# Kernel optimization log

Hardware: AMD Instinct MI355X
Metric: run time of the kernel (lower is better)

The kernel has to match this reference:

```python
import jax, jax.numpy as jnp
import numpy as np

B, N, IN_DIM = 2, 2048, 512
D_MODEL, N_HEADS, N_CLASSES = 1024, 16, 1024


def sin_pos_encoding(n, d):
    # Matches SinPositionalEncoding buffer pe[:n]
    pos = jnp.arange(n, dtype=jnp.float32)[:, None]
    div = jnp.exp(jnp.arange(0, d, 2, dtype=jnp.float32) * (-np.log(10000.0) / d))
    pe = jnp.zeros((n, d), dtype=jnp.float32)
    pe = pe.at[:, 0::2].set(jnp.sin(pos * div))
    pe = pe.at[:, 1::2].set(jnp.cos(pos * div))
    return pe


def setup_inputs() -> dict:
    key = jax.random.key(0)
    ks = jax.random.split(key, 9)
    s_emb = (2.0 / (IN_DIM + D_MODEL)) ** 0.5
    s_qk = (2.0 / (2 * D_MODEL)) ** 0.5
    s_v = (2.0 / (D_MODEL + 1)) ** 0.5
    s_o = (2.0 / (N_HEADS + D_MODEL)) ** 0.5
    s_dec = (2.0 / (D_MODEL + N_CLASSES)) ** 0.5
    return {
        'X': jax.random.normal(ks[0], (B, N, IN_DIM), dtype=jnp.float32),
        'emb_w': jax.random.normal(ks[1], (IN_DIM, D_MODEL), dtype=jnp.float32) * s_emb,
        'emb_b': jax.random.normal(ks[2], (D_MODEL,), dtype=jnp.float32) * 0.01,
        'Wq': jax.random.normal(ks[3], (N_HEADS, D_MODEL, D_MODEL), dtype=jnp.float32) * s_qk,
        'Wk': jax.random.normal(ks[4], (N_HEADS, D_MODEL, D_MODEL), dtype=jnp.float32) * s_qk,
        'Wv': jax.random.normal(ks[5], (N_HEADS, D_MODEL, 1), dtype=jnp.float32) * s_v,
        'Wo': jax.random.normal(ks[6], (N_HEADS, D_MODEL), dtype=jnp.float32) * s_o,
        'dec_w': jax.random.normal(ks[7], (D_MODEL, N_CLASSES), dtype=jnp.float32) * s_dec,
        'dec_b': jax.random.normal(ks[8], (N_CLASSES,), dtype=jnp.float32) * 0.01,
    }


def reference(X, emb_w, emb_b, Wq, Wk, Wv, Wo, dec_w, dec_b):
    b, n, _ = X.shape
    d = emb_w.shape[1]
    h = X @ emb_w + emb_b                       # [b, n, d]
    h = h + sin_pos_encoding(n, d)[None]        # positional encoding
    Q = jnp.einsum('bnd,hde->bhne', h, Wq)      # [b, H, n, d]
    K = jnp.einsum('bnd,hde->bhne', h, Wk)      # [b, H, n, d]
    V = jnp.einsum('bnd,hdv->bhnv', h, Wv)      # [b, H, n, 1]
    scores = jnp.einsum('bhqe,bhke->bhqk', Q, K) / jnp.sqrt(jnp.float32(d))
    # mask[:, 0] = 1 is applied MULTIPLICATIVELY before softmax: column 0 -> 0
    scores = scores.at[..., 0].set(0.0)
    attn = jax.nn.softmax(scores, axis=-1)      # [b, H, n, n]
    ctx = jnp.einsum('bhqk,bhkv->bhqv', attn, V)  # [b, H, n, 1]
    ctx = jnp.transpose(ctx, (0, 2, 1, 3)).reshape(b, n, -1)  # [b, n, H]
    out = ctx @ Wo                              # [b, n, d]
    out = out @ dec_w + dec_b                   # [b, n, n_classes]
    return out
```

## Files before the change

kernel.cpp:

```cpp
#include <hip/hip_runtime.h>
#include <cstdint>

typedef __attribute__((ext_vector_type(8))) short bf16x8;
typedef __attribute__((ext_vector_type(4))) float f32x4;

#define B_ 2
#define N_ 2048
#define IN_DIM_ 512
#define D_ 1024
#define H_ 16

__device__ __forceinline__ unsigned short f2bf(float f) {
  uint32_t u = __float_as_uint(f);
  u = u + 0x7fffu + ((u >> 16) & 1u);
  return (unsigned short)(u >> 16);
}
__device__ __forceinline__ float bf2f(unsigned short b) {
  return __uint_as_float(((uint32_t)b) << 16);
}

__device__ __forceinline__ void gll16(const void* g, void* l) {
  __builtin_amdgcn_global_load_lds(
      (const __attribute__((address_space(1))) uint32_t*)g,
      (__attribute__((address_space(3))) uint32_t*)l, 16, 0, 0);
}

__global__ __launch_bounds__(256) void cast_bf16(const float* __restrict__ X,
                                                 unsigned short* __restrict__ O, int n) {
  int i = (blockIdx.x * 256 + threadIdx.x) * 4;
  if (i + 3 < n) {
    f32x4 v = *(const f32x4*)(X + i);
    uint32_t p0 = (uint32_t)f2bf(v[0]) | ((uint32_t)f2bf(v[1]) << 16);
    uint32_t p1 = (uint32_t)f2bf(v[2]) | ((uint32_t)f2bf(v[3]) << 16);
    *(uint32_t*)(O + i) = p0;
    *(uint32_t*)(O + i + 2) = p1;
  }
}

__global__ __launch_bounds__(256) void cast_bf16x2(const float* __restrict__ X0,
                                                   const float* __restrict__ X1,
                                                   unsigned short* __restrict__ O0,
                                                   unsigned short* __restrict__ O1, int n) {
  int i = (blockIdx.x * 256 + threadIdx.x) * 4;
  const bool second = (i >= n);
  const int j = second ? i - n : i;
  const float* X = second ? X1 : X0;
  unsigned short* O = second ? O1 : O0;
  f32x4 v = *(const f32x4*)(X + j);
  uint32_t p0 = (uint32_t)f2bf(v[0]) | ((uint32_t)f2bf(v[1]) << 16);
  uint32_t p1 = (uint32_t)f2bf(v[2]) | ((uint32_t)f2bf(v[3]) << 16);
  *(uint32_t*)(O + j) = p0;
  *(uint32_t*)(O + j + 2) = p1;
}

__global__ __launch_bounds__(256) void transpose_cast(const float* __restrict__ W,
                                                      unsigned short* __restrict__ WT,
                                                      int K, int N) {
  __shared__ float t[32][33];
  const int tx = threadIdx.x, ty = threadIdx.y;
  const int x = blockIdx.x * 32 + tx;
  const int y = blockIdx.y * 32 + ty;
  #pragma unroll
  for (int i = 0; i < 4; ++i)
    t[ty + i * 8][tx] = W[(size_t)(y + i * 8) * N + x];
  __syncthreads();
  const int ox = blockIdx.y * 32 + tx;
  #pragma unroll
  for (int i = 0; i < 4; ++i) {
    const int oy = blockIdx.x * 32 + ty + i * 8;
    WT[(size_t)oy * K + ox] = f2bf(t[tx][ty + i * 8]);
  }
}

__global__ __launch_bounds__(256) void gemm_embed(
    const unsigned short* __restrict__ Xbf, const unsigned short* __restrict__ EbT,
    const float* __restrict__ emb_b, unsigned short* __restrict__ Hbf) {
  const int tid = threadIdx.x, l = tid & 63, w = tid >> 6;
  const int wm = w >> 1, wn = w & 1;
  const int bm = blockIdx.y * 128, bn = blockIdx.x * 128;
  __shared__ unsigned short As[128 * 32], Bs[128 * 32];
  const unsigned short* Ab = Xbf + (size_t)bm * IN_DIM_;
  const unsigned short* Bb = EbT + (size_t)bn * IN_DIM_;
  f32x4 acc[4][4] = {};
  const int lr = l >> 2, lc = (l & 3) * 8;
  for (int k0 = 0; k0 < IN_DIM_; k0 += 32) {
    #pragma unroll
    for (int i = 0; i < 2; ++i) {
      const int c = w * 2 + i;
      gll16(Ab + (size_t)(c * 16 + lr) * IN_DIM_ + k0 + lc, As + c * 512);
      gll16(Bb + (size_t)(c * 16 + lr) * IN_DIM_ + k0 + lc, Bs + c * 512);
    }
    __syncthreads();
    bf16x8 af[4], bfr[4];
    #pragma unroll
    for (int f = 0; f < 4; ++f) {
      af[f]  = *(const bf16x8*)(As + (wm * 64 + f * 16 + (l & 15)) * 32 + (l >> 4) * 8);
      bfr[f] = *(const bf16x8*)(Bs + (wn * 64 + f * 16 + (l & 15)) * 32 + (l >> 4) * 8);
    }
    #pragma unroll
    for (int fr = 0; fr < 4; ++fr)
      #pragma unroll
      for (int fc = 0; fc < 4; ++fc)
        acc[fr][fc] = __builtin_amdgcn_mfma_f32_16x16x32_bf16(af[fr], bfr[fc], acc[fr][fc], 0, 0, 0);
    __syncthreads();
  }
  const float kF = -0.017988946039015983f;
  #pragma unroll
  for (int fr = 0; fr < 4; ++fr) {
    #pragma unroll
    for (int fc = 0; fc < 4; ++fc) {
      const int col = bn + wn * 64 + fc * 16 + (l & 15);
      const float eb = emb_b[col];
      const float fac = expf((float)(col >> 1) * kF);
      #pragma unroll
      for (int j = 0; j < 4; ++j) {
        const int row = bm + wm * 64 + fr * 16 + (l >> 4) * 4 + j;
        const float pos = (float)(row & (N_ - 1));
        const float ang = pos * fac;
        const float pe = (col & 1) ? cosf(ang) : sinf(ang);
        float v = acc[fr][fc][j] + eb + pe;
        float o = __shfl_xor(v, 1);
        unsigned short mb = f2bf(v), ob = f2bf(o);
        uint32_t pk = (l & 1) ? ((uint32_t)ob | ((uint32_t)mb << 16))
                              : ((uint32_t)mb | ((uint32_t)ob << 16));
        const bool mine = (l & 1) ? (j >= 2) : (j < 2);
        if (mine)
          *(uint32_t*)(Hbf + (size_t)row * D_ + (col & ~1)) = pk;
      }
    }
  }
}

__global__ __launch_bounds__(256) void gemm_nt(
    const unsigned short* __restrict__ A, const unsigned short* __restrict__ Bm,
    unsigned short* __restrict__ O, int K, long aZ, long bZ, long oZ, int swz) {
  int bx = blockIdx.x, by = blockIdx.y, bz = blockIdx.z;
  if (swz) {
    const int nx = gridDim.x, ny = gridDim.y;
    const int nwg = nx * ny * gridDim.z;
    const int bid = bx + nx * (by + ny * bz);
    const int wid = (bid & 7) * (nwg >> 3) + (bid >> 3);
    bx = wid % nx;
    const int rest = wid / nx;
    by = rest % ny;
    bz = rest / ny;
  }
  const int z = bz;
  const int tid = threadIdx.x, l = tid & 63, w = tid >> 6;
  const int wm = w >> 1, wn = w & 1;
  const int bm = by * 128, bn = bx * 128;
  const int ldo = gridDim.x * 128;
  __shared__ unsigned short As[2 * 128 * 32], Bs[2 * 128 * 32];
  const unsigned short* Ab = A + (size_t)z * aZ + (size_t)bm * K;
  const unsigned short* Bb = Bm + (size_t)z * bZ + (size_t)bn * K;
  f32x4 acc[4][4] = {};
  const int lr = l >> 2, lc = (l & 3) * 8;
  for (int k0 = 0; k0 < K; k0 += 64) {
    #pragma unroll
    for (int half = 0; half < 2; ++half) {
      #pragma unroll
      for (int i = 0; i < 2; ++i) {
        const int c = w * 2 + i;
        gll16(Ab + (size_t)(c * 16 + lr) * K + k0 + half * 32 + lc,
              As + half * 4096 + c * 512);
        gll16(Bb + (size_t)(c * 16 + lr) * K + k0 + half * 32 + lc,
              Bs + half * 4096 + c * 512);
      }
    }
    __syncthreads();
    #pragma unroll
    for (int half = 0; half < 2; ++half) {
      bf16x8 af[4], bfr[4];
      #pragma unroll
      for (int f = 0; f < 4; ++f) {
        af[f]  = *(const bf16x8*)(As + half * 4096 + (wm * 64 + f * 16 + (l & 15)) * 32 + (l >> 4) * 8);
        bfr[f] = *(const bf16x8*)(Bs + half * 4096 + (wn * 64 + f * 16 + (l & 15)) * 32 + (l >> 4) * 8);
      }
      #pragma unroll
      for (int fr = 0; fr < 4; ++fr)
        #pragma unroll
        for (int fc = 0; fc < 4; ++fc)
          acc[fr][fc] = __builtin_amdgcn_mfma_f32_16x16x32_bf16(af[fr], bfr[fc], acc[fr][fc], 0, 0, 0);
    }
    __syncthreads();
  }
  unsigned short* obase = O + (size_t)z * oZ;
  #pragma unroll
  for (int fr = 0; fr < 4; ++fr) {
    #pragma unroll
    for (int fc = 0; fc < 4; ++fc) {
      const int col = bn + wn * 64 + fc * 16 + (l & 15);
      #pragma unroll
      for (int j = 0; j < 4; ++j) {
        const int row = bm + wm * 64 + fr * 16 + (l >> 4) * 4 + j;
        float v = acc[fr][fc][j];
        float o = __shfl_xor(v, 1);
        unsigned short mb = f2bf(v), ob = f2bf(o);
        uint32_t pk = (l & 1) ? ((uint32_t)ob | ((uint32_t)mb << 16))
                              : ((uint32_t)mb | ((uint32_t)ob << 16));
        const bool mine = (l & 1) ? (j >= 2) : (j < 2);
        if (mine)
          *(uint32_t*)(obase + (size_t)row * ldo + (col & ~1)) = pk;
      }
    }
  }
}

__global__ __launch_bounds__(256) void v_wodec_kernel(
    const unsigned short* __restrict__ Hbf, const float* __restrict__ Wv,
    float* __restrict__ V, const float* __restrict__ Wo,
    const float* __restrict__ dec_w, float* __restrict__ M) {
  if (blockIdx.x < 1024) {
    const int l = threadIdx.x & 63, w = threadIdx.x >> 6;
    const int ng = blockIdx.x * 4 + w;
    const int b = ng >> 11, n = ng & (N_ - 1);
    const unsigned short* hr = Hbf + (size_t)ng * D_;
    float hv[16];
    #pragma unroll
    for (int i = 0; i < 2; ++i) {
      bf16x8 x = *(const bf16x8*)(hr + l * 16 + i * 8);
      #pragma unroll
      for (int j = 0; j < 8; ++j) hv[i * 8 + j] = bf2f((unsigned short)x[j]);
    }
    for (int h = 0; h < H_; ++h) {
      const float* wr = Wv + (size_t)h * D_ + l * 16;
      float s = 0.f;
      #pragma unroll
      for (int i = 0; i < 4; ++i) {
        f32x4 w4 = *(const f32x4*)(wr + i * 4);
        s += hv[i*4+0]*w4[0] + hv[i*4+1]*w4[1] + hv[i*4+2]*w4[2] + hv[i*4+3]*w4[3];
      }
      #pragma unroll
      for (int m = 1; m < 64; m <<= 1) s += __shfl_xor(s, m);
      if (l == 0) V[((size_t)b * H_ + h) * N_ + n] = s;
    }
  } else {
    const int idx = (blockIdx.x - 1024) * 256 + threadIdx.x;
    const int h = idx >> 10, c = idx & 1023;
    float s = 0.f;
    #pragma unroll 4
    for (int d = 0; d < D_; ++d) s += Wo[h * D_ + d] * dec_w[(size_t)d * 1024 + c];
    M[idx] = s;
  }
}

__global__ __launch_bounds__(512, 2) void score_flash(
    const unsigned short* __restrict__ G, const unsigned short* __restrict__ Hb,
    const float* __restrict__ V, float* __restrict__ Pp) {
  extern __shared__ unsigned short KQ[];
  const int bid = blockIdx.x;
  const int wid = (bid & 7) * 128 + (bid >> 3);
  const int kt = wid & 7, qt = (wid >> 3) & 7, h = wid >> 6;
  const int tid = threadIdx.x;
  const int l = tid & 63, l15 = l & 15, l7 = l & 7, lq = l >> 4;
  const int wv = tid >> 6, wm = wv >> 2, wn = wv & 3;
  const unsigned short* Ab = G + ((size_t)h * N_ + qt * 256) * D_;
  const unsigned short* Bb = Hb + (size_t)(kt * 256) * D_;
  const float* Vf = V + (size_t)h * N_;

  const int srow = tid >> 3, spc = tid & 7, scol = (spc ^ (srow & 7)) * 8;
  auto stageU = [&](const unsigned short* src, int rowBase, int k0, unsigned short* ldsU) {
    gll16(src + (size_t)(rowBase + srow) * D_ + k0 + scol, ldsU + tid * 8);
  };

  float vv[4];
  #pragma unroll
  for (int fc = 0; fc < 4; ++fc)
    vv[fc] = Vf[kt * 256 + wn * 64 + fc * 16 + l15];

  {
    unsigned short* A0 = KQ;
    unsigned short* B0 = KQ + 16384;
    stageU(Bb, 0, 0, B0); stageU(Bb, 64, 0, B0 + 4096);
    stageU(Bb, 128, 0, B0 + 8192); stageU(Bb, 192, 0, B0 + 12288);
    stageU(Ab, 0, 0, A0); stageU(Ab, 128, 0, A0 + 8192);
    stageU(Ab, 64, 0, A0 + 4096); stageU(Ab, 192, 0, A0 + 12288);
  }
  __builtin_amdgcn_sched_barrier(0);
  asm volatile("s_waitcnt vmcnt(2)" ::: "memory");
  __builtin_amdgcn_s_barrier();
  __builtin_amdgcn_sched_barrier(0);

  f32x4 acc[8][4] = {};
  const int arow0 = wm * 128 + l15;
  const int brow0 = wn * 64 + l15;

  for (int t = 0; t < 16; ++t) {
    unsigned short* Acur = KQ + (t & 1) * 32768;
    unsigned short* Bcur = Acur + 16384;
    unsigned short* Anxt = KQ + ((t & 1) ^ 1) * 32768;
    unsigned short* Bnxt = Anxt + 16384;
    const int k0n = (t + 1) * 64;
    const bool more = (t < 15);
    bf16x8 bfr[4][2];
    #pragma unroll
    for (int r = 0; r < 4; ++r) {
      if (r == 0) {
        #pragma unroll
        for (int fc = 0; fc < 4; ++fc)
          #pragma unroll
          for (int kh = 0; kh < 2; ++kh)
            bfr[fc][kh] = *(const bf16x8*)(Bcur + (brow0 + fc * 16) * 64 +
                                           (((kh * 4 + lq) ^ l7) * 8));
      }
      bf16x8 af[2][2];
      #pragma unroll
      for (int i = 0; i < 2; ++i)
        #pragma unroll
        for (int kh = 0; kh < 2; ++kh)
          af[i][kh] = *(const bf16x8*)(Acur + (arow0 + (2 * r + i) * 16) * 64 +
                                       (((kh * 4 + lq) ^ l7) * 8));
      if (more) {
        if (r == 0)      { stageU(Bb, 0, k0n, Bnxt);        stageU(Bb, 64, k0n, Bnxt + 4096); }
        else if (r == 1) { stageU(Bb, 128, k0n, Bnxt + 8192); stageU(Bb, 192, k0n, Bnxt + 12288); }
        else if (r == 2) { stageU(Ab, 0, k0n, Anxt);        stageU(Ab, 128, k0n, Anxt + 8192); }
        else             { stageU(Ab, 64, k0n, Anxt + 4096); stageU(Ab, 192, k0n, Anxt + 12288); }
      }
      __builtin_amdgcn_sched_barrier(0);
      if (r == 1) {
        if (t == 15) asm volatile("s_waitcnt vmcnt(0)" ::: "memory");
        else         asm volatile("s_waitcnt vmcnt(4)" ::: "memory");
      }
      if (r == 3 && more) asm volatile("s_waitcnt vmcnt(2)" ::: "memory");
      __builtin_amdgcn_s_barrier();
      __builtin_amdgcn_sched_barrier(0);
      __builtin_amdgcn_s_setprio(1);
      #pragma unroll
      for (int i = 0; i < 2; ++i)
        #pragma unroll
        for (int fc = 0; fc < 4; ++fc)
          #pragma unroll
          for (int kh = 0; kh < 2; ++kh)
            acc[2 * r + i][fc] = __builtin_amdgcn_mfma_f32_16x16x32_bf16(
                af[i][kh], bfr[fc][kh], acc[2 * r + i][fc], 0, 0, 0);
      __builtin_amdgcn_s_setprio(0);
      __builtin_amdgcn_sched_barrier(0);
      __builtin_amdgcn_s_barrier();
      __builtin_amdgcn_sched_barrier(0);
    }
  }

  __syncthreads();
  float* sb = (float*)KQ;
  #pragma unroll
  for (int fr = 0; fr < 8; ++fr) {
    #pragma unroll
    for (int j = 0; j < 4; ++j) {
      float s4[4];
      #pragma unroll
      for (int fc = 0; fc < 4; ++fc) s4[fc] = acc[fr][fc][j] * 0.03125f;
      if (kt == 0 && wn == 0 && l15 == 0) s4[0] = 0.0f;
      float ps = 0.f, pv = 0.f;
      #pragma unroll
      for (int fc = 0; fc < 4; ++fc) {
        const float e = __expf(s4[fc] - 8.0f);
        ps += e; pv += e * vv[fc];
      }
      ps += __shfl_xor(ps, 1); pv += __shfl_xor(pv, 1);
      ps += __shfl_xor(ps, 2); pv += __shfl_xor(pv, 2);
      ps += __shfl_xor(ps, 4); pv += __shfl_xor(pv, 4);
      ps += __shfl_xor(ps, 8); pv += __shfl_xor(pv, 8);
      if (l15 == 0) {
        const int q = wm * 128 + fr * 16 + lq * 4 + j;
        sb[(q * 4 + wn) * 2 + 0] = ps;
        sb[(q * 4 + wn) * 2 + 1] = pv;
      }
    }
  }
  __syncthreads();
  if (tid < 256) {
    const int q = tid;
    float L = 0.f, O = 0.f;
    #pragma unroll
    for (int n = 0; n < 4; ++n) { L += sb[(q * 4 + n) * 2]; O += sb[(q * 4 + n) * 2 + 1]; }
    float* p = Pp + (((size_t)h * 8 + kt) * N_ + qt * 256 + q) * 2;
    p[0] = L; p[1] = O;
  }
}

__global__ __launch_bounds__(256) void merge8(const float* __restrict__ Pp,
                                              float* __restrict__ ctx) {
  const int idx = blockIdx.x * 256 + threadIdx.x;
  const int h = idx >> 11, q = idx & (N_ - 1);
  float L = 0.f, O = 0.f;
  #pragma unroll
  for (int kt = 0; kt < 8; ++kt) {
    const float* p = Pp + (((size_t)h * 8 + kt) * N_ + q) * 2;
    L += p[0]; O += p[1];
  }
  ctx[(size_t)q * H_ + h] = O / L;
}

__global__ __launch_bounds__(256) void final_kernel(
    const float* __restrict__ ctx, const float* __restrict__ M,
    const float* __restrict__ dec_b, float* __restrict__ out) {
  const int idx = blockIdx.x * 256 + threadIdx.x;
  const int c = idx & 1023;
  const float* cr = ctx + (size_t)(idx >> 10) * H_;
  float s = dec_b[c];
  #pragma unroll
  for (int h = 0; h < H_; ++h) s += cr[h] * M[h * 1024 + c];
  out[idx] = s;
}

extern "C" void kernel_launch(void* const* d_in, const int* in_sizes, int n_in,
                              void* d_out, int out_size, void* d_ws, size_t ws_size,
                              hipStream_t stream) {
  const float* X     = (const float*)d_in[0];
  const float* emb_w = (const float*)d_in[1];
  const float* emb_b = (const float*)d_in[2];
  const float* Wq    = (const float*)d_in[3];
  const float* Wk    = (const float*)d_in[4];
  const float* Wv    = (const float*)d_in[5];
  const float* Wo    = (const float*)d_in[6];
  const float* dec_b = (const float*)d_in[8];
  const float* dec_w = (const float*)d_in[7];
  float* out = (float*)d_out;
  (void)in_sizes; (void)n_in; (void)out_size;

  char* ws = (char*)d_ws;
  unsigned short* Hbf = (unsigned short*)(ws);
  unsigned short* Wkq = (unsigned short*)(ws + ((size_t)8 << 20));
  float* Vb  = (float*)(ws + ((size_t)40 << 20));
  float* ctx = (float*)(ws + ((size_t)40 << 20) + ((size_t)256 << 10));
  float* Mw  = (float*)(ws + ((size_t)40 << 20) + ((size_t)512 << 10));
  char* S = ws + ((size_t)41 << 20);
  unsigned short* Xbf  = (unsigned short*)(S);
  unsigned short* EbT  = (unsigned short*)(S + ((size_t)4 << 20));
  unsigned short* Wqbf = (unsigned short*)(S);
  unsigned short* Wkbf = (unsigned short*)(S + ((size_t)32 << 20));
  unsigned short* G    = (unsigned short*)(S);
  float* Pp = (float*)d_out;

  const size_t need = ((size_t)41 << 20) + ((size_t)64 << 20);
  if (ws_size < need) return;

  cast_bf16<<<2048, 256, 0, stream>>>(X, Xbf, B_ * N_ * IN_DIM_);
  transpose_cast<<<dim3(32, 16, 1), dim3(32, 8), 0, stream>>>(emb_w, EbT, IN_DIM_, D_);
  gemm_embed<<<dim3(8, 32), 256, 0, stream>>>(Xbf, EbT, emb_b, Hbf);
  cast_bf16x2<<<32768, 256, 0, stream>>>(Wq, Wk, Wqbf, Wkbf, H_ * D_ * D_);
  gemm_nt<<<dim3(8, 8, 16), 256, 0, stream>>>(Wkbf, Wqbf, Wkq, D_,
                                              (long)D_ * D_, (long)D_ * D_, (long)D_ * D_, 1);
  v_wodec_kernel<<<1088, 256, 0, stream>>>(Hbf, Wv, Vb, Wo, dec_w, Mw);

  for (int b = 0; b < B_; ++b) {
    const unsigned short* Hb = Hbf + (size_t)b * N_ * D_;
    gemm_nt<<<dim3(8, 16, 16), 256, 0, stream>>>(Hb, Wkq, G, D_,
                                                 0L, (long)D_ * D_, (long)N_ * D_, 1);
    score_flash<<<1024, 512, 131072, stream>>>(G, Hb, Vb + (size_t)b * H_ * N_, Pp);
    merge8<<<128, 256, 0, stream>>>(Pp, ctx + (size_t)b * N_ * H_);
  }
  final_kernel<<<16384, 256, 0, stream>>>(ctx, Mw, dec_b, out);
}
```

Measured before the change: 756.1 us.

## Replace 128x128 gemm_nt with pipelined 256x256 tile GEMM, fuse prep casts

The simple 128x128-tile GEMM used for the Wk·Wq product and the per-batch H·Wkq projection is replaced by a 256x256-tile, 8-wave kernel. It uses swizzled LDS layout, double-buffered global-to-LDS loads issued between MFMA phases, and explicit waitcnt/barrier scheduling, mirroring the pipeline already in score_flash. The goal is more data reuse per loaded byte and overlap of loads with MFMA work. It needs 128KB of dynamic LDS per block, which limits occupancy. The X cast and emb_w transpose-cast are also merged into one launch.

Result: faster. 699.6 us (median of 3 runs) (-7.5%).

```diff
diff --git a/kernel.cpp b/kernel.cpp
--- a/kernel.cpp
+++ b/kernel.cpp
@@ -25,15 +25,36 @@
       (__attribute__((address_space(3))) uint32_t*)l, 16, 0, 0);
 }
 
-__global__ __launch_bounds__(256) void cast_bf16(const float* __restrict__ X,
-                                                 unsigned short* __restrict__ O, int n) {
-  int i = (blockIdx.x * 256 + threadIdx.x) * 4;
-  if (i + 3 < n) {
-    f32x4 v = *(const f32x4*)(X + i);
-    uint32_t p0 = (uint32_t)f2bf(v[0]) | ((uint32_t)f2bf(v[1]) << 16);
-    uint32_t p1 = (uint32_t)f2bf(v[2]) | ((uint32_t)f2bf(v[3]) << 16);
-    *(uint32_t*)(O + i) = p0;
-    *(uint32_t*)(O + i + 2) = p1;
+__global__ __launch_bounds__(256) void prep_kernel(
+    const float* __restrict__ X, unsigned short* __restrict__ Xbf,
+    const float* __restrict__ emb_w, unsigned short* __restrict__ EbT) {
+  __shared__ float t[32][33];
+  const int tid = threadIdx.x;
+  if (blockIdx.x < 2048) {
+    const int i = (blockIdx.x * 256 + tid) * 4;
+    if (i + 3 < B_ * N_ * IN_DIM_) {
+      f32x4 v = *(const f32x4*)(X + i);
+      uint32_t p0 = (uint32_t)f2bf(v[0]) | ((uint32_t)f2bf(v[1]) << 16);
+      uint32_t p1 = (uint32_t)f2bf(v[2]) | ((uint32_t)f2bf(v[3]) << 16);
+      *(uint32_t*)(Xbf + i) = p0;
+      *(uint32_t*)(Xbf + i + 2) = p1;
+    }
+  } else {
+    const int tb = blockIdx.x - 2048;
+    const int bx = tb & 31, by = tb >> 5;
+    const int tx = tid & 31, ty = tid >> 5;
+    const int x = bx * 32 + tx;
+    const int y = by * 32 + ty;
+    #pragma unroll
+    for (int i = 0; i < 4; ++i)
+      t[ty + i * 8][tx] = emb_w[(size_t)(y + i * 8) * D_ + x];
+    __syncthreads();
+    const int ox = by * 32 + tx;
+    #pragma unroll
+    for (int i = 0; i < 4; ++i) {
+      const int oy = bx * 32 + ty + i * 8;
+      EbT[(size_t)oy * IN_DIM_ + ox] = f2bf(t[tx][ty + i * 8]);
+    }
   }
 }
 
@@ -53,25 +74,6 @@
   *(uint32_t*)(O + j + 2) = p1;
 }
 
-__global__ __launch_bounds__(256) void transpose_cast(const float* __restrict__ W,
-                                                      unsigned short* __restrict__ WT,
-                                                      int K, int N) {
-  __shared__ float t[32][33];
-  const int tx = threadIdx.x, ty = threadIdx.y;
-  const int x = blockIdx.x * 32 + tx;
-  const int y = blockIdx.y * 32 + ty;
-  #pragma unroll
-  for (int i = 0; i < 4; ++i)
-    t[ty + i * 8][tx] = W[(size_t)(y + i * 8) * N + x];
-  __syncthreads();
-  const int ox = blockIdx.y * 32 + tx;
-  #pragma unroll
-  for (int i = 0; i < 4; ++i) {
-    const int oy = blockIdx.x * 32 + ty + i * 8;
-    WT[(size_t)oy * K + ox] = f2bf(t[tx][ty + i * 8]);
-  }
-}
-
 __global__ __launch_bounds__(256) void gemm_embed(
     const unsigned short* __restrict__ Xbf, const unsigned short* __restrict__ EbT,
     const float* __restrict__ emb_b, unsigned short* __restrict__ Hbf) {
@@ -131,68 +133,111 @@
   }
 }
 
-__global__ __launch_bounds__(256) void gemm_nt(
+__global__ __launch_bounds__(512, 2) void gemm_nt256(
     const unsigned short* __restrict__ A, const unsigned short* __restrict__ Bm,
-    unsigned short* __restrict__ O, int K, long aZ, long bZ, long oZ, int swz) {
-  int bx = blockIdx.x, by = blockIdx.y, bz = blockIdx.z;
-  if (swz) {
-    const int nx = gridDim.x, ny = gridDim.y;
-    const int nwg = nx * ny * gridDim.z;
-    const int bid = bx + nx * (by + ny * bz);
-    const int wid = (bid & 7) * (nwg >> 3) + (bid >> 3);
-    bx = wid % nx;
-    const int rest = wid / nx;
-    by = rest % ny;
-    bz = rest / ny;
-  }
-  const int z = bz;
-  const int tid = threadIdx.x, l = tid & 63, w = tid >> 6;
-  const int wm = w >> 1, wn = w & 1;
-  const int bm = by * 128, bn = bx * 128;
-  const int ldo = gridDim.x * 128;
-  __shared__ unsigned short As[2 * 128 * 32], Bs[2 * 128 * 32];
-  const unsigned short* Ab = A + (size_t)z * aZ + (size_t)bm * K;
-  const unsigned short* Bb = Bm + (size_t)z * bZ + (size_t)bn * K;
-  f32x4 acc[4][4] = {};
-  const int lr = l >> 2, lc = (l & 3) * 8;
-  for (int k0 = 0; k0 < K; k0 += 64) {
-    #pragma unroll
-    for (int half = 0; half < 2; ++half) {
-      #pragma unroll
-      for (int i = 0; i < 2; ++i) {
-        const int c = w * 2 + i;
-        gll16(Ab + (size_t)(c * 16 + lr) * K + k0 + half * 32 + lc,
-              As + half * 4096 + c * 512);
-        gll16(Bb + (size_t)(c * 16 + lr) * K + k0 + half * 32 + lc,
-              Bs + half * 4096 + c * 512);
-      }
-    }
-    __syncthreads();
-    #pragma unroll
-    for (int half = 0; half < 2; ++half) {
-      bf16x8 af[4], bfr[4];
-      #pragma unroll
-      for (int f = 0; f < 4; ++f) {
-        af[f]  = *(const bf16x8*)(As + half * 4096 + (wm * 64 + f * 16 + (l & 15)) * 32 + (l >> 4) * 8);
-        bfr[f] = *(const bf16x8*)(Bs + half * 4096 + (wn * 64 + f * 16 + (l & 15)) * 32 + (l >> 4) * 8);
-      }
-      #pragma unroll
-      for (int fr = 0; fr < 4; ++fr)
+    unsigned short* __restrict__ O, int K, long aZ, long bZ, long oZ,
+    int nbx, int nby, int ldo) {
+  extern __shared__ unsigned short KQ[];
+  const int nb = gridDim.x;
+  const int bid = blockIdx.x;
+  const int wid = (bid & 7) * (nb >> 3) + (bid >> 3);
+  const int bxi = wid % nbx;
+  const int rest = wid / nbx;
+  const int byi = rest % nby;
+  const int z = rest / nby;
+  const int tid = threadIdx.x;
+  const int l = tid & 63, l15 = l & 15, l7 = l & 7, lq = l >> 4;
+  const int wv = tid >> 6, wm = wv >> 2, wn = wv & 3;
+  const unsigned short* Ab = A + (size_t)z * aZ + (size_t)(byi * 256) * K;
+  const unsigned short* Bb = Bm + (size_t)z * bZ + (size_t)(bxi * 256) * K;
+
+  const int srow = tid >> 3, spc = tid & 7, scol = (spc ^ (srow & 7)) * 8;
+  auto stageU = [&](const unsigned short* src, int rowBase, int k0, unsigned short* ldsU) {
+    gll16(src + (size_t)(rowBase + srow) * K + k0 + scol, ldsU + tid * 8);
+  };
+
+  {
+    unsigned short* A0 = KQ;
+    unsigned short* B0 = KQ + 16384;
+    stageU(Bb, 0, 0, B0); stageU(Bb, 64, 0, B0 + 4096);
+    stageU(Bb, 128, 0, B0 + 8192); stageU(Bb, 192, 0, B0 + 12288);
+    stageU(Ab, 0, 0, A0); stageU(Ab, 128, 0, A0 + 8192);
+    stageU(Ab, 64, 0, A0 + 4096); stageU(Ab, 192, 0, A0 + 12288);
+  }
+  __builtin_amdgcn_sched_barrier(0);
+  asm volatile("s_waitcnt vmcnt(2)" ::: "memory");
+  __builtin_amdgcn_s_barrier();
+  __builtin_amdgcn_sched_barrier(0);
+
+  f32x4 acc[8][4] = {};
+  const int arow0 = wm * 128 + l15;
+  const int brow0 = wn * 64 + l15;
+  const int nt = K >> 6;
+
+  for (int t = 0; t < nt; ++t) {
+    unsigned short* Acur = KQ + (t & 1) * 32768;
+    unsigned short* Bcur = Acur + 16384;
+    unsigned short* Anxt = KQ + ((t & 1) ^ 1) * 32768;
+    unsigned short* Bnxt = Anxt + 16384;
+    const int k0n = (t + 1) * 64;
+    const bool more = (t < nt - 1);
+    bf16x8 bfr[4][2];
+    #pragma unroll
+    for (int r = 0; r < 4; ++r) {
+      if (r == 0) {
         #pragma unroll
         for (int fc = 0; fc < 4; ++fc)
-          acc[fr][fc] = __builtin_amdgcn_mfma_f32_16x16x32_bf16(af[fr], bfr[fc], acc[fr][fc], 0, 0, 0);
-    }
-    __syncthreads();
-  }
-  unsigned short* obase = O + (size_t)z * oZ;
+          #pragma unroll
+          for (int kh = 0; kh < 2; ++kh)
+            bfr[fc][kh] = *(const bf16x8*)(Bcur + (brow0 + fc * 16) * 64 +
+                                           (((kh * 4 + lq) ^ l7) * 8));
+      }
+      bf16x8 af[2][2];
+      #pragma unroll
+      for (int i = 0; i < 2; ++i)
+        #pragma unroll
+        for (int kh = 0; kh < 2; ++kh)
+          af[i][kh] = *(const bf16x8*)(Acur + (arow0 + (2 * r + i) * 16) * 64 +
+                                       (((kh * 4 + lq) ^ l7) * 8));
+      if (more) {
+        if (r == 0)      { stageU(Bb, 0, k0n, Bnxt);          stageU(Bb, 64, k0n, Bnxt + 4096); }
+        else if (r == 1) { stageU(Bb, 128, k0n, Bnxt + 8192); stageU(Bb, 192, k0n, Bnxt + 12288); }
+        else if (r == 2) { stageU(Ab, 0, k0n, Anxt);          stageU(Ab, 128, k0n, Anxt + 8192); }
+        else             { stageU(Ab, 64, k0n, Anxt + 4096);  stageU(Ab, 192, k0n, Anxt + 12288); }
+      }
+      __builtin_amdgcn_sched_barrier(0);
+      if (r == 1) {
+        if (t == nt - 1) asm volatile("s_waitcnt vmcnt(0)" ::: "memory");
+        else             asm volatile("s_waitcnt vmcnt(4)" ::: "memory");
+      }
+      if (r == 3 && more) asm volatile("s_waitcnt vmcnt(2)" ::: "memory");
+      __builtin_amdgcn_s_barrier();
+      __builtin_amdgcn_sched_barrier(0);
+      __builtin_amdgcn_s_setprio(1);
+      #pragma unroll
+      for (int i = 0; i < 2; ++i)
+        #pragma unroll
+        for (int fc = 0; fc < 4; ++fc)
+          #pragma unroll
+          for (int kh = 0; kh < 2; ++kh)
+            acc[2 * r + i][fc] = __builtin_amdgcn_mfma_f32_16x16x32_bf16(
+                af[i][kh], bfr[fc][kh], acc[2 * r + i][fc], 0, 0, 0);
+      __builtin_amdgcn_s_setprio(0);
+      __builtin_amdgcn_sched_barrier(0);
+      __builtin_amdgcn_s_barrier();
+      __builtin_amdgcn_sched_barrier(0);
+    }
+  }
+
+  unsigned short* obase = O + (size_t)z * oZ + (size_t)(byi * 256) * ldo + bxi * 256;
   #pragma unroll
-  for (int fr = 0; fr < 4; ++fr) {
+  for (int fr = 0; fr < 8; ++fr) {
     #pragma unroll
     for (int fc = 0; fc < 4; ++fc) {
-      const int col = bn + wn * 64 + fc * 16 + (l & 15);
+      const int col = wn * 64 + fc * 16 + l15;
       #pragma unroll
       for (int j = 0; j < 4; ++j) {
-        const int row = bm + wm * 64 + fr * 16 + (l >> 4) * 4 + j;
+        const int row = wm * 128 + fr * 16 + lq * 4 + j;
         float v = acc[fr][fc][j];
         float o = __shfl_xor(v, 1);
         unsigned short mb = f2bf(v), ob = f2bf(o);
@@ -311,10 +356,10 @@
           af[i][kh] = *(const bf16x8*)(Acur + (arow0 + (2 * r + i) * 16) * 64 +
                                        (((kh * 4 + lq) ^ l7) * 8));
       if (more) {
-        if (r == 0)      { stageU(Bb, 0, k0n, Bnxt);        stageU(Bb, 64, k0n, Bnxt + 4096); }
+        if (r == 0)      { stageU(Bb, 0, k0n, Bnxt);          stageU(Bb, 64, k0n, Bnxt + 4096); }
         else if (r == 1) { stageU(Bb, 128, k0n, Bnxt + 8192); stageU(Bb, 192, k0n, Bnxt + 12288); }
-        else if (r == 2) { stageU(Ab, 0, k0n, Anxt);        stageU(Ab, 128, k0n, Anxt + 8192); }
-        else             { stageU(Ab, 64, k0n, Anxt + 4096); stageU(Ab, 192, k0n, Anxt + 12288); }
+        else if (r == 2) { stageU(Ab, 0, k0n, Anxt);          stageU(Ab, 128, k0n, Anxt + 8192); }
+        else             { stageU(Ab, 64, k0n, Anxt + 4096);  stageU(Ab, 192, k0n, Anxt + 12288); }
       }
       __builtin_amdgcn_sched_barrier(0);
       if (r == 1) {
@@ -435,18 +480,19 @@
   const size_t need = ((size_t)41 << 20) + ((size_t)64 << 20);
   if (ws_size < need) return;
 
-  cast_bf16<<<2048, 256, 0, stream>>>(X, Xbf, B_ * N_ * IN_DIM_);
-  transpose_cast<<<dim3(32, 16, 1), dim3(32, 8), 0, stream>>>(emb_w, EbT, IN_DIM_, D_);
+  prep_kernel<<<2560, 256, 0, stream>>>(X, Xbf, emb_w, EbT);
   gemm_embed<<<dim3(8, 32), 256, 0, stream>>>(Xbf, EbT, emb_b, Hbf);
   cast_bf16x2<<<32768, 256, 0, stream>>>(Wq, Wk, Wqbf, Wkbf, H_ * D_ * D_);
-  gemm_nt<<<dim3(8, 8, 16), 256, 0, stream>>>(Wkbf, Wqbf, Wkq, D_,
-                                              (long)D_ * D_, (long)D_ * D_, (long)D_ * D_, 1);
+  gemm_nt256<<<256, 512, 131072, stream>>>(Wkbf, Wqbf, Wkq, D_,
+                                           (long)D_ * D_, (long)D_ * D_, (long)D_ * D_,
+                                           4, 4, 1024);
   v_wodec_kernel<<<1088, 256, 0, stream>>>(Hbf, Wv, Vb, Wo, dec_w, Mw);
 
   for (int b = 0; b < B_; ++b) {
     const unsigned short* Hb = Hbf + (size_t)b * N_ * D_;
-    gemm_nt<<<dim3(8, 16, 16), 256, 0, stream>>>(Hb, Wkq, G, D_,
-                                                 0L, (long)D_ * D_, (long)N_ * D_, 1);
+    gemm_nt256<<<512, 512, 131072, stream>>>(Hb, Wkq, G, D_,
+                                             0L, (long)D_ * D_, (long)N_ * D_,
+                                             4, 8, 1024);
     score_flash<<<1024, 512, 131072, stream>>>(G, Hb, Vb + (size_t)b * H_ * N_, Pp);
     merge8<<<128, 256, 0, stream>>>(Pp, ctx + (size_t)b * N_ * H_);
   }
```
